# Performance work log

Hardware: AMD Instinct MI355X
Metric: run time of the kernel (lower is better)

Reference implementation:

```python
import jax, jax.numpy as jnp
import numpy as np

B, N, C = 2, 2048, 1024
H = 16
D = C // H
HID = 4 * C
EPS = 1e-5


def layernorm(x, g, b):
    mu = jnp.mean(x, axis=-1, keepdims=True)
    var = jnp.var(x, axis=-1, keepdims=True)
    return (x - mu) * jax.lax.rsqrt(var + EPS) * g + b


def setup_inputs() -> dict:
    key = jax.random.key(0)
    ks = jax.random.split(key, 8)
    s = lambda fan_in: 1.0 / np.sqrt(fan_in)
    return {
        "x": jax.random.normal(ks[0], (B, N, C), dtype=jnp.float32),
        "ln1_g": jnp.ones((C,), jnp.float32),
        "ln1_b": jnp.zeros((C,), jnp.float32),
        "w_qkv": jax.random.normal(ks[1], (C, 3 * C), jnp.float32) * s(C),
        "w_proj": jax.random.normal(ks[2], (C, C), jnp.float32) * s(C),
        "b_proj": jnp.zeros((C,), jnp.float32),
        "ln2_g": jnp.ones((C,), jnp.float32),
        "ln2_b": jnp.zeros((C,), jnp.float32),
        "w_fc1": jax.random.normal(ks[3], (C, HID), jnp.float32) * s(C),
        "b_fc1": jnp.zeros((HID,), jnp.float32),
        "w_fc2": jax.random.normal(ks[4], (HID, C), jnp.float32) * s(HID),
        "b_fc2": jnp.zeros((C,), jnp.float32),
        "metadata": 0,
        "thw_shape": 2048,
    }


def reference(x, ln1_g, ln1_b, w_qkv, w_proj, b_proj, ln2_g, ln2_b,
              w_fc1, b_fc1, w_fc2, b_fc2, metadata, thw_shape):
    scale = 1.0 / np.sqrt(D)
    # --- attention branch (pre-norm) ---
    xn = layernorm(x, ln1_g, ln1_b)
    qkv = (xn @ w_qkv).reshape(B, N, 3, H, D)
    q = jnp.transpose(qkv[:, :, 0], (0, 2, 1, 3))  # [B,H,N,D]
    k = jnp.transpose(qkv[:, :, 1], (0, 2, 1, 3))
    v = jnp.transpose(qkv[:, :, 2], (0, 2, 1, 3))
    attn = jax.nn.softmax(jnp.einsum('bhnd,bhmd->bhnm', q, k) * scale, axis=-1)
    o = jnp.einsum('bhnm,bhmd->bhnd', attn, v)
    o = jnp.transpose(o, (0, 2, 1, 3)).reshape(B, N, C)
    x = x + (o @ w_proj + b_proj)
    # --- MLP branch (pre-norm) ---
    xn2 = layernorm(x, ln2_g, ln2_b)
    h = jax.nn.gelu(xn2 @ w_fc1 + b_fc1, approximate=False)  # torch GELU = exact erf
    x = x + (h @ w_fc2 + b_fc2)
    return x
```

## Files before the change

kernel.cpp:

```cpp
#include <hip/hip_runtime.h>

#define B_   2
#define N_   2048
#define C_   1024
#define H_   16
#define D_   64
#define HID_ 4096
#define M_   (B_ * N_)

typedef __attribute__((ext_vector_type(8))) short bf16x8;
typedef __attribute__((ext_vector_type(4))) short short4v;
typedef __attribute__((ext_vector_type(4))) float f32x4;

__device__ __forceinline__ unsigned short f2bf(float f) {
  unsigned int u = __builtin_bit_cast(unsigned int, f);
  u += 0x7fffu + ((u >> 16) & 1u);
  return (unsigned short)(u >> 16);
}

__device__ __forceinline__ void gl2lds16(const void* g, void* l) {
  __builtin_amdgcn_global_load_lds(
      (const __attribute__((address_space(1))) unsigned int*)g,
      (__attribute__((address_space(3))) unsigned int*)l, 16, 0, 0);
}

__global__ __launch_bounds__(256) void ln_kernel(const float* __restrict__ x,
                                                 const float* __restrict__ g,
                                                 const float* __restrict__ bta,
                                                 unsigned short* __restrict__ out) {
  int row  = blockIdx.x * 4 + (threadIdx.x >> 6);
  int lane = threadIdx.x & 63;
  const float* xr = x + (size_t)row * C_;
  float4 v[4];
  float s1 = 0.f, s2 = 0.f;
#pragma unroll
  for (int j = 0; j < 4; j++) {
    v[j] = *(const float4*)(xr + j * 256 + lane * 4);
    s1 += v[j].x + v[j].y + v[j].z + v[j].w;
    s2 += v[j].x * v[j].x + v[j].y * v[j].y + v[j].z * v[j].z + v[j].w * v[j].w;
  }
#pragma unroll
  for (int m = 1; m < 64; m <<= 1) { s1 += __shfl_xor(s1, m); s2 += __shfl_xor(s2, m); }
  float mu  = s1 * (1.0f / C_);
  float var = s2 * (1.0f / C_) - mu * mu;
  float rs  = rsqrtf(var + 1e-5f);
#pragma unroll
  for (int j = 0; j < 4; j++) {
    const float4 gv = *(const float4*)(g + j * 256 + lane * 4);
    const float4 bv = *(const float4*)(bta + j * 256 + lane * 4);
    ushort4 o;
    o.x = f2bf((v[j].x - mu) * rs * gv.x + bv.x);
    o.y = f2bf((v[j].y - mu) * rs * gv.y + bv.y);
    o.z = f2bf((v[j].z - mu) * rs * gv.z + bv.z);
    o.w = f2bf((v[j].w - mu) * rs * gv.w + bv.w);
    *(ushort4*)(out + (size_t)row * C_ + j * 256 + lane * 4) = o;
  }
}

__global__ __launch_bounds__(256) void wtrans_kernel(const float* __restrict__ W,
                                                     unsigned short* __restrict__ Wt,
                                                     int K, int N) {
  __shared__ float t[32][33];
  int n0 = blockIdx.x * 32, k0 = blockIdx.y * 32;
  int tx = threadIdx.x, ty = threadIdx.y;
#pragma unroll
  for (int j = 0; j < 4; j++)
    t[ty + j * 8][tx] = W[(size_t)(k0 + ty + j * 8) * N + n0 + tx];
  __syncthreads();
#pragma unroll
  for (int j = 0; j < 4; j++)
    Wt[(size_t)(n0 + ty + j * 8) * K + k0 + tx] = f2bf(t[tx][ty + j * 8]);
}

__global__ __launch_bounds__(256) void vtrans_kernel(const unsigned short* __restrict__ v,
                                                     unsigned short* __restrict__ vt) {
  __shared__ unsigned short t[32][33];
  int bh = blockIdx.z;
  int n0 = blockIdx.x * 32, d0 = blockIdx.y * 32;
  const unsigned short* src = v + (size_t)bh * N_ * D_;
  unsigned short* dst = vt + (size_t)bh * D_ * N_;
  int tx = threadIdx.x, ty = threadIdx.y;
#pragma unroll
  for (int j = 0; j < 4; j++)
    t[ty + j * 8][tx] = src[(size_t)(n0 + ty + j * 8) * D_ + d0 + tx];
  __syncthreads();
#pragma unroll
  for (int j = 0; j < 4; j++)
    dst[(size_t)(d0 + ty + j * 8) * N_ + n0 + tx] = t[tx][ty + j * 8];
}

template <int MODE, int BN>
__global__ __launch_bounds__(256) void gemm_kernel(
    const unsigned short* __restrict__ A,
    const unsigned short* __restrict__ Wt,
    const float* __restrict__ bias,
    const float* __restrict__ resid,
    float* __restrict__ outf,
    unsigned short* __restrict__ outb0,
    unsigned short* __restrict__ outb1,
    unsigned short* __restrict__ outb2,
    int M, int N, int K) {
  constexpr int MT = (BN == 128) ? 4 : 2;
  __shared__ __align__(16) short As[128][64];
  __shared__ __align__(16) short Bs[BN][64];
  int tid = threadIdx.x;
  int w = tid >> 6, lane = tid & 63, r = lane & 15, quad = lane >> 4;
  int rowbase = (BN == 128) ? (w >> 1) * 64 : w * 32;
  int colbase = (BN == 128) ? (w & 1) * 64 : 0;
  int bM = blockIdx.y * 128, bN = blockIdx.x * BN;

  int srow   = (w << 3) + (lane >> 3);
  int schunk = (lane & 7) ^ ((lane >> 3) & 7);
  const unsigned short* aP = A  + (size_t)(bM + srow) * K + schunk * 8;
  const unsigned short* bP = Wt + (size_t)(bN + srow) * K + schunk * 8;

  int pc0 = (quad ^ (r & 7)) * 8;

  f32x4 acc[MT][4];
#pragma unroll
  for (int i = 0; i < MT; i++)
#pragma unroll
    for (int j = 0; j < 4; j++) acc[i][j] = f32x4{0.f, 0.f, 0.f, 0.f};

  for (int k0 = 0; k0 < K; k0 += 64) {
    __syncthreads();
#pragma unroll
    for (int p = 0; p < 4; p++)
      gl2lds16(aP + (size_t)(p * 32) * K + k0, &As[p * 32 + (w << 3)][0]);
#pragma unroll
    for (int p = 0; p < BN / 32; p++)
      gl2lds16(bP + (size_t)(p * 32) * K + k0, &Bs[p * 32 + (w << 3)][0]);
    __syncthreads();
#pragma unroll
    for (int kh = 0; kh < 2; kh++) {
      int pc = pc0 ^ (kh * 32);
      bf16x8 af[MT], bfr[4];
#pragma unroll
      for (int mt = 0; mt < MT; mt++)
        af[mt] = *(const bf16x8*)&As[rowbase + mt * 16 + r][pc];
#pragma unroll
      for (int nt = 0; nt < 4; nt++)
        bfr[nt] = *(const bf16x8*)&Bs[colbase + nt * 16 + r][pc];
#pragma unroll
      for (int mt = 0; mt < MT; mt++)
#pragma unroll
        for (int nt = 0; nt < 4; nt++)
          acc[mt][nt] = __builtin_amdgcn_mfma_f32_16x16x32_bf16(af[mt], bfr[nt], acc[mt][nt], 0, 0, 0);
    }
  }

#pragma unroll
  for (int mt = 0; mt < MT; mt++) {
#pragma unroll
    for (int nt = 0; nt < 4; nt++) {
#pragma unroll
      for (int i = 0; i < 4; i++) {
        int gm = bM + rowbase + mt * 16 + quad * 4 + i;
        int gn = bN + colbase + nt * 16 + r;
        float val = acc[mt][nt][i];
        if (MODE == 0) {
          int s = gn >> 10, c = gn & 1023;
          int hh = c >> 6, d = c & 63;
          int b = gm >> 11, n = gm & 2047;
          size_t di = ((size_t)(b * H_ + hh) * N_ + n) * D_ + d;
          unsigned short bvv = f2bf(s == 0 ? val * 0.125f : val);
          (s == 0 ? outb0 : (s == 1 ? outb1 : outb2))[di] = bvv;
        } else if (MODE == 1) {
          outf[(size_t)gm * N + gn] = val + bias[gn] + resid[(size_t)gm * N + gn];
        } else {
          float t = val + bias[gn];
          float gl = 0.5f * t * (1.0f + erff(t * 0.70710678118f));
          outb0[(size_t)gm * N + gn] = f2bf(gl);
        }
      }
    }
  }
}

__global__ __launch_bounds__(256) void attn_kernel(const unsigned short* __restrict__ qb,
                                                   const unsigned short* __restrict__ kb,
                                                   const unsigned short* __restrict__ vtb,
                                                   unsigned short* __restrict__ ob) {
  __shared__ __align__(16) short Ks[128][64];
  __shared__ __align__(16) short Vts[64][128];
  int tid = threadIdx.x;
  int w = tid >> 6, lane = tid & 63, r = lane & 15, quad = lane >> 4;
  int bh = blockIdx.x >> 4, qt = blockIdx.x & 15;
  const unsigned short* qh  = qb  + (size_t)bh * N_ * D_;
  const unsigned short* kh  = kb  + (size_t)bh * N_ * D_;
  const unsigned short* vth = vtb + (size_t)bh * D_ * N_;

  bf16x8 qf[2][2];
#pragma unroll
  for (int mt = 0; mt < 2; mt++)
#pragma unroll
    for (int ks = 0; ks < 2; ks++)
      qf[mt][ks] = *(const bf16x8*)(qh + (size_t)(qt * 128 + w * 32 + mt * 16 + r) * D_ + ks * 32 + quad * 8);

  float mst[2] = {-1e30f, -1e30f}, lst[2] = {0.f, 0.f};
  f32x4 oacc[2][4];
#pragma unroll
  for (int mt = 0; mt < 2; mt++)
#pragma unroll
    for (int nt = 0; nt < 4; nt++) oacc[mt][nt] = f32x4{0.f, 0.f, 0.f, 0.f};

  int krow   = (w << 3) + (lane >> 3);
  int kchunk = (lane & 7) ^ ((lane >> 3) & 7);
  const unsigned short* kP = kh + (size_t)krow * D_ + kchunk * 8;
  int vrow   = (w << 2) + (lane >> 4);
  int vchunk = (lane & 15) ^ (vrow & 7);
  const unsigned short* vP = vth + (size_t)vrow * N_ + vchunk * 8;

  short* Plw = &Ks[0][0] + w * 2048;
  int swz = (r & 7);

  for (int t = 0; t < 16; t++) {
    __syncthreads();
#pragma unroll
    for (int p = 0; p < 4; p++)
      gl2lds16(kP + (size_t)(t * 128 + p * 32) * D_, &Ks[p * 32 + (w << 3)][0]);
#pragma unroll
    for (int p = 0; p < 4; p++)
      gl2lds16(vP + (size_t)(p * 16) * N_ + t * 128, &Vts[p * 16 + (w << 2)][0]);
    __syncthreads();

    f32x4 sacc[2][8];
#pragma unroll
    for (int mt = 0; mt < 2; mt++)
#pragma unroll
      for (int nt = 0; nt < 8; nt++) sacc[mt][nt] = f32x4{0.f, 0.f, 0.f, 0.f};
#pragma unroll
    for (int ks = 0; ks < 2; ks++) {
#pragma unroll
      for (int nt = 0; nt < 8; nt++) {
        bf16x8 kfr = *(const bf16x8*)&Ks[nt * 16 + r][((ks * 4 + quad) ^ swz) * 8];
#pragma unroll
        for (int mt = 0; mt < 2; mt++)
          sacc[mt][nt] = __builtin_amdgcn_mfma_f32_16x16x32_bf16(kfr, qf[mt][ks], sacc[mt][nt], 0, 0, 0);
      }
    }

    float alpha[2];
#pragma unroll
    for (int mt = 0; mt < 2; mt++) {
      float tm = -1e30f;
#pragma unroll
      for (int nt = 0; nt < 8; nt++)
#pragma unroll
        for (int i = 0; i < 4; i++) tm = fmaxf(tm, sacc[mt][nt][i]);
      tm = fmaxf(tm, __shfl_xor(tm, 16));
      tm = fmaxf(tm, __shfl_xor(tm, 32));
      float mnew = fmaxf(mst[mt], tm);
      alpha[mt] = __expf(mst[mt] - mnew);
      mst[mt] = mnew;
      float rs = 0.f;
#pragma unroll
      for (int nt = 0; nt < 8; nt++)
#pragma unroll
        for (int i = 0; i < 4; i++) {
          float p = __expf(sacc[mt][nt][i] - mnew);
          sacc[mt][nt][i] = p;
          rs += p;
        }
      rs += __shfl_xor(rs, 16);
      rs += __shfl_xor(rs, 32);
      lst[mt] = lst[mt] * alpha[mt] + rs;
#pragma unroll
      for (int i = 0; i < 4; i++) {
        float av = __shfl(alpha[mt], (lane & 48) | (quad * 4 + i));
#pragma unroll
        for (int nt = 0; nt < 4; nt++) oacc[mt][nt][i] *= av;
      }
    }

    __syncthreads();

#pragma unroll
    for (int mt = 0; mt < 2; mt++) {
#pragma unroll
      for (int nt = 0; nt < 8; nt++) {
        short4v pk;
        pk[0] = (short)f2bf(sacc[mt][nt][0]);
        pk[1] = (short)f2bf(sacc[mt][nt][1]);
        pk[2] = (short)f2bf(sacc[mt][nt][2]);
        pk[3] = (short)f2bf(sacc[mt][nt][3]);
        *(short4v*)&Plw[r * 128 + (((nt * 2 + (quad >> 1)) ^ swz) * 8) + (quad & 1) * 4] = pk;
      }
      asm volatile("" ::: "memory");
#pragma unroll
      for (int ks = 0; ks < 4; ks++) {
        bf16x8 pfr = *(const bf16x8*)&Plw[r * 128 + ((ks * 4 + quad) ^ swz) * 8];
#pragma unroll
        for (int nt2 = 0; nt2 < 4; nt2++) {
          bf16x8 vfr = *(const bf16x8*)&Vts[nt2 * 16 + r][((ks * 4 + quad) ^ swz) * 8];
          oacc[mt][nt2] = __builtin_amdgcn_mfma_f32_16x16x32_bf16(pfr, vfr, oacc[mt][nt2], 0, 0, 0);
        }
      }
      asm volatile("" ::: "memory");
    }
  }

  int bb = bh >> 4, hh = bh & 15;
#pragma unroll
  for (int mt = 0; mt < 2; mt++) {
#pragma unroll
    for (int i = 0; i < 4; i++) {
      float li = __shfl(lst[mt], (lane & 48) | (quad * 4 + i));
      float inv = 1.0f / li;
      int row = qt * 128 + w * 32 + mt * 16 + quad * 4 + i;
#pragma unroll
      for (int nt2 = 0; nt2 < 4; nt2++) {
        int d = nt2 * 16 + r;
        ob[((size_t)bb * N_ + row) * C_ + hh * D_ + d] = f2bf(oacc[mt][nt2][i] * inv);
      }
    }
  }
}

extern "C" void kernel_launch(void* const* d_in, const int* in_sizes, int n_in,
                              void* d_out, int out_size, void* d_ws, size_t ws_size,
                              hipStream_t stream) {
  const float* x     = (const float*)d_in[0];
  const float* ln1g  = (const float*)d_in[1];
  const float* ln1b  = (const float*)d_in[2];
  const float* wqkv  = (const float*)d_in[3];
  const float* wproj = (const float*)d_in[4];
  const float* bproj = (const float*)d_in[5];
  const float* ln2g  = (const float*)d_in[6];
  const float* ln2b  = (const float*)d_in[7];
  const float* wfc1  = (const float*)d_in[8];
  const float* bfc1  = (const float*)d_in[9];
  const float* wfc2  = (const float*)d_in[10];
  const float* bfc2  = (const float*)d_in[11];
  float* out = (float*)d_out;

  const size_t MB = 1u << 20;
  if (ws_size < 88 * MB) return;
  char* w = (char*)d_ws;
  unsigned short* xn    = (unsigned short*)(w + 0 * MB);
  unsigned short* qbuf  = (unsigned short*)(w + 8 * MB);
  unsigned short* kbuf  = (unsigned short*)(w + 16 * MB);
  unsigned short* vbuf  = (unsigned short*)(w + 24 * MB);
  unsigned short* hbuf  = (unsigned short*)(w + 0 * MB);
  unsigned short* obuf  = (unsigned short*)(w + 32 * MB);
  float*          x2    = (float*)         (w + 40 * MB);
  unsigned short* xn2   = (unsigned short*)(w + 56 * MB);
  unsigned short* vtb   = (unsigned short*)(w + 56 * MB);
  unsigned short* wqkvt = (unsigned short*)(w + 64 * MB);
  unsigned short* wprjt = (unsigned short*)(w + 70 * MB);
  unsigned short* wfc1t = (unsigned short*)(w + 72 * MB);
  unsigned short* wfc2t = (unsigned short*)(w + 80 * MB);

  dim3 tb(32, 8);
  ln_kernel<<<M_ / 4, 256, 0, stream>>>(x, ln1g, ln1b, xn);
  wtrans_kernel<<<dim3(3 * C_ / 32, C_ / 32), tb, 0, stream>>>(wqkv, wqkvt, C_, 3 * C_);
  wtrans_kernel<<<dim3(C_ / 32, C_ / 32), tb, 0, stream>>>(wproj, wprjt, C_, C_);
  wtrans_kernel<<<dim3(HID_ / 32, C_ / 32), tb, 0, stream>>>(wfc1, wfc1t, C_, HID_);
  wtrans_kernel<<<dim3(C_ / 32, HID_ / 32), tb, 0, stream>>>(wfc2, wfc2t, HID_, C_);

  gemm_kernel<0, 128><<<dim3(3 * C_ / 128, M_ / 128), 256, 0, stream>>>(
      xn, wqkvt, nullptr, nullptr, nullptr, qbuf, kbuf, vbuf, M_, 3 * C_, C_);
  vtrans_kernel<<<dim3(N_ / 32, D_ / 32, B_ * H_), tb, 0, stream>>>(vbuf, vtb);
  attn_kernel<<<B_ * H_ * (N_ / 128), 256, 0, stream>>>(qbuf, kbuf, vtb, obuf);
  gemm_kernel<1, 64><<<dim3(C_ / 64, M_ / 128), 256, 0, stream>>>(
      obuf, wprjt, bproj, x, x2, nullptr, nullptr, nullptr, M_, C_, C_);
  ln_kernel<<<M_ / 4, 256, 0, stream>>>(x2, ln2g, ln2b, xn2);
  gemm_kernel<2, 128><<<dim3(HID_ / 128, M_ / 128), 256, 0, stream>>>(
      xn2, wfc1t, bfc1, nullptr, nullptr, hbuf, nullptr, nullptr, M_, HID_, C_);
  gemm_kernel<1, 64><<<dim3(C_ / 64, M_ / 128), 256, 0, stream>>>(
      hbuf, wfc2t, bfc2, x2, out, nullptr, nullptr, nullptr, M_, C_, HID_);
}
```

Baseline: 385.1 us.

## Split attention KV range and FC2 K dimension across blocks for more parallelism

Attention now splits each query tile's key range into two halves processed by separate blocks. Each block writes a normalized partial output plus its running max and sum, and a new combine kernel merges the halves with log-sum-exp weights. The FC2 GEMM switches to 128-wide tiles with a two-way split-K; one half writes bias plus residual and the other writes a partial buffer that a separate add kernel folds in. Both changes aim to fill more CUs on a grid that was small (512 attention blocks, 512 FC2 blocks), at the cost of extra kernel launches, intermediate traffic, and an extra bf16 rounding of the partial attention outputs.

```diff
diff --git a/kernel.cpp b/kernel.cpp
--- a/kernel.cpp
+++ b/kernel.cpp
@@ -16,6 +16,10 @@
   unsigned int u = __builtin_bit_cast(unsigned int, f);
   u += 0x7fffu + ((u >> 16) & 1u);
   return (unsigned short)(u >> 16);
+}
+__device__ __forceinline__ float bf2f(unsigned short s) {
+  unsigned int u = ((unsigned int)s) << 16;
+  return __builtin_bit_cast(float, u);
 }
 
 __device__ __forceinline__ void gl2lds16(const void* g, void* l) {
@@ -96,6 +100,7 @@
     const float* __restrict__ bias,
     const float* __restrict__ resid,
     float* __restrict__ outf,
+    float* __restrict__ partf,
     unsigned short* __restrict__ outb0,
     unsigned short* __restrict__ outb1,
     unsigned short* __restrict__ outb2,
@@ -109,6 +114,10 @@
   int colbase = (BN == 128) ? (w & 1) * 64 : 0;
   int bM = blockIdx.y * 128, bN = blockIdx.x * BN;
 
+  int kz   = (MODE == 3) ? blockIdx.z : 0;
+  int kbeg = (MODE == 3) ? kz * (K >> 1) : 0;
+  int kend = (MODE == 3) ? kbeg + (K >> 1) : K;
+
   int srow   = (w << 3) + (lane >> 3);
   int schunk = (lane & 7) ^ ((lane >> 3) & 7);
   const unsigned short* aP = A  + (size_t)(bM + srow) * K + schunk * 8;
@@ -122,7 +131,7 @@
 #pragma unroll
     for (int j = 0; j < 4; j++) acc[i][j] = f32x4{0.f, 0.f, 0.f, 0.f};
 
-  for (int k0 = 0; k0 < K; k0 += 64) {
+  for (int k0 = kbeg; k0 < kend; k0 += 64) {
     __syncthreads();
 #pragma unroll
     for (int p = 0; p < 4; p++)
@@ -167,25 +176,42 @@
           (s == 0 ? outb0 : (s == 1 ? outb1 : outb2))[di] = bvv;
         } else if (MODE == 1) {
           outf[(size_t)gm * N + gn] = val + bias[gn] + resid[(size_t)gm * N + gn];
-        } else {
+        } else if (MODE == 2) {
           float t = val + bias[gn];
           float gl = 0.5f * t * (1.0f + erff(t * 0.70710678118f));
           outb0[(size_t)gm * N + gn] = f2bf(gl);
+        } else {
+          if (kz == 0)
+            outf[(size_t)gm * N + gn] = val + bias[gn] + resid[(size_t)gm * N + gn];
+          else
+            partf[(size_t)gm * N + gn] = val;
         }
       }
     }
   }
 }
 
-__global__ __launch_bounds__(256) void attn_kernel(const unsigned short* __restrict__ qb,
-                                                   const unsigned short* __restrict__ kb,
-                                                   const unsigned short* __restrict__ vtb,
-                                                   unsigned short* __restrict__ ob) {
+__global__ __launch_bounds__(256) void addpart_kernel(float* __restrict__ out,
+                                                      const float* __restrict__ part) {
+  int i = blockIdx.x * 256 + threadIdx.x;
+  float4 a = *(const float4*)(out + (size_t)i * 4);
+  float4 b = *(const float4*)(part + (size_t)i * 4);
+  a.x += b.x; a.y += b.y; a.z += b.z; a.w += b.w;
+  *(float4*)(out + (size_t)i * 4) = a;
+}
+
+__global__ __launch_bounds__(256, 4) void attn_kernel(const unsigned short* __restrict__ qb,
+                                                      const unsigned short* __restrict__ kb,
+                                                      const unsigned short* __restrict__ vtb,
+                                                      unsigned short* __restrict__ Op,
+                                                      float2* __restrict__ ml) {
   __shared__ __align__(16) short Ks[128][64];
   __shared__ __align__(16) short Vts[64][128];
   int tid = threadIdx.x;
   int w = tid >> 6, lane = tid & 63, r = lane & 15, quad = lane >> 4;
-  int bh = blockIdx.x >> 4, qt = blockIdx.x & 15;
+  int kbi = blockIdx.x & 1;
+  int idx = blockIdx.x >> 1;
+  int bh = idx >> 4, qt = idx & 15;
   const unsigned short* qh  = qb  + (size_t)bh * N_ * D_;
   const unsigned short* kh  = kb  + (size_t)bh * N_ * D_;
   const unsigned short* vth = vtb + (size_t)bh * D_ * N_;
@@ -214,7 +240,7 @@
   short* Plw = &Ks[0][0] + w * 2048;
   int swz = (r & 7);
 
-  for (int t = 0; t < 16; t++) {
+  for (int t = kbi * 8; t < kbi * 8 + 8; t++) {
     __syncthreads();
 #pragma unroll
     for (int p = 0; p < 4; p++)
@@ -300,9 +326,13 @@
     }
   }
 
-  int bb = bh >> 4, hh = bh & 15;
+  size_t base = ((size_t)(kbi * 32 + bh)) * N_;
 #pragma unroll
   for (int mt = 0; mt < 2; mt++) {
+    if (quad == 0) {
+      int row = qt * 128 + w * 32 + mt * 16 + r;
+      ml[base + row] = float2{mst[mt], lst[mt]};
+    }
 #pragma unroll
     for (int i = 0; i < 4; i++) {
       float li = __shfl(lst[mt], (lane & 48) | (quad * 4 + i));
@@ -311,10 +341,43 @@
 #pragma unroll
       for (int nt2 = 0; nt2 < 4; nt2++) {
         int d = nt2 * 16 + r;
-        ob[((size_t)bb * N_ + row) * C_ + hh * D_ + d] = f2bf(oacc[mt][nt2][i] * inv);
-      }
-    }
-  }
+        Op[(base + row) * D_ + d] = f2bf(oacc[mt][nt2][i] * inv);
+      }
+    }
+  }
+}
+
+__global__ __launch_bounds__(256) void attn_combine_kernel(const unsigned short* __restrict__ Op,
+                                                           const float2* __restrict__ ml,
+                                                           unsigned short* __restrict__ ob) {
+  int gid = blockIdx.x * 256 + threadIdx.x;
+  int row = gid >> 3;
+  int dq  = (gid & 7) << 3;
+  int bh = row >> 11, n = row & 2047;
+  int bb = bh >> 4, hh = bh & 15;
+  float2 a0 = ml[row];
+  float2 a1 = ml[(size_t)B_ * H_ * N_ + row];
+  float m = fmaxf(a0.x, a1.x);
+  float w0 = __expf(a0.x - m) * a0.y;
+  float w1 = __expf(a1.x - m) * a1.y;
+  float inv = 1.0f / (w0 + w1);
+  w0 *= inv; w1 *= inv;
+  const ushort4 o0  = *(const ushort4*)(Op + (size_t)row * D_ + dq);
+  const ushort4 o0b = *(const ushort4*)(Op + (size_t)row * D_ + dq + 4);
+  const ushort4 o1  = *(const ushort4*)(Op + ((size_t)B_ * H_ * N_ + row) * D_ + dq);
+  const ushort4 o1b = *(const ushort4*)(Op + ((size_t)B_ * H_ * N_ + row) * D_ + dq + 4);
+  ushort4 r0, r1;
+  r0.x = f2bf(w0 * bf2f(o0.x) + w1 * bf2f(o1.x));
+  r0.y = f2bf(w0 * bf2f(o0.y) + w1 * bf2f(o1.y));
+  r0.z = f2bf(w0 * bf2f(o0.z) + w1 * bf2f(o1.z));
+  r0.w = f2bf(w0 * bf2f(o0.w) + w1 * bf2f(o1.w));
+  r1.x = f2bf(w0 * bf2f(o0b.x) + w1 * bf2f(o1b.x));
+  r1.y = f2bf(w0 * bf2f(o0b.y) + w1 * bf2f(o1b.y));
+  r1.z = f2bf(w0 * bf2f(o0b.z) + w1 * bf2f(o1b.z));
+  r1.w = f2bf(w0 * bf2f(o0b.w) + w1 * bf2f(o1b.w));
+  unsigned short* dst = ob + ((size_t)bb * N_ + n) * C_ + hh * D_ + dq;
+  *(ushort4*)dst = r0;
+  *(ushort4*)(dst + 4) = r1;
 }
 
 extern "C" void kernel_launch(void* const* d_in, const int* in_sizes, int n_in,
@@ -338,15 +401,18 @@
   if (ws_size < 88 * MB) return;
   char* w = (char*)d_ws;
   unsigned short* xn    = (unsigned short*)(w + 0 * MB);
+  float2*         mlbuf = (float2*)        (w + 0 * MB);
   unsigned short* qbuf  = (unsigned short*)(w + 8 * MB);
   unsigned short* kbuf  = (unsigned short*)(w + 16 * MB);
   unsigned short* vbuf  = (unsigned short*)(w + 24 * MB);
   unsigned short* hbuf  = (unsigned short*)(w + 0 * MB);
   unsigned short* obuf  = (unsigned short*)(w + 32 * MB);
   float*          x2    = (float*)         (w + 40 * MB);
+  unsigned short* opart = (unsigned short*)(w + 40 * MB);
   unsigned short* xn2   = (unsigned short*)(w + 56 * MB);
   unsigned short* vtb   = (unsigned short*)(w + 56 * MB);
   unsigned short* wqkvt = (unsigned short*)(w + 64 * MB);
+  float*          partf = (float*)         (w + 64 * MB);
   unsigned short* wprjt = (unsigned short*)(w + 70 * MB);
   unsigned short* wfc1t = (unsigned short*)(w + 72 * MB);
   unsigned short* wfc2t = (unsigned short*)(w + 80 * MB);
@@ -359,14 +425,16 @@
   wtrans_kernel<<<dim3(C_ / 32, HID_ / 32), tb, 0, stream>>>(wfc2, wfc2t, HID_, C_);
 
   gemm_kernel<0, 128><<<dim3(3 * C_ / 128, M_ / 128), 256, 0, stream>>>(
-      xn, wqkvt, nullptr, nullptr, nullptr, qbuf, kbuf, vbuf, M_, 3 * C_, C_);
+      xn, wqkvt, nullptr, nullptr, nullptr, nullptr, qbuf, kbuf, vbuf, M_, 3 * C_, C_);
   vtrans_kernel<<<dim3(N_ / 32, D_ / 32, B_ * H_), tb, 0, stream>>>(vbuf, vtb);
-  attn_kernel<<<B_ * H_ * (N_ / 128), 256, 0, stream>>>(qbuf, kbuf, vtb, obuf);
+  attn_kernel<<<B_ * H_ * (N_ / 128) * 2, 256, 0, stream>>>(qbuf, kbuf, vtb, opart, mlbuf);
+  attn_combine_kernel<<<B_ * H_ * N_ * 8 / 256, 256, 0, stream>>>(opart, mlbuf, obuf);
   gemm_kernel<1, 64><<<dim3(C_ / 64, M_ / 128), 256, 0, stream>>>(
-      obuf, wprjt, bproj, x, x2, nullptr, nullptr, nullptr, M_, C_, C_);
+      obuf, wprjt, bproj, x, x2, nullptr, nullptr, nullptr, nullptr, M_, C_, C_);
   ln_kernel<<<M_ / 4, 256, 0, stream>>>(x2, ln2g, ln2b, xn2);
   gemm_kernel<2, 128><<<dim3(HID_ / 128, M_ / 128), 256, 0, stream>>>(
-      xn2, wfc1t, bfc1, nullptr, nullptr, hbuf, nullptr, nullptr, M_, HID_, C_);
-  gemm_kernel<1, 64><<<dim3(C_ / 64, M_ / 128), 256, 0, stream>>>(
-      hbuf, wfc2t, bfc2, x2, out, nullptr, nullptr, nullptr, M_, C_, HID_);
-}
+      xn2, wfc1t, bfc1, nullptr, nullptr, nullptr, hbuf, nullptr, nullptr, M_, HID_, C_);
+  gemm_kernel<3, 128><<<dim3(C_ / 128, M_ / 128, 2), 256, 0, stream>>>(
+      hbuf, wfc2t, bfc2, x2, out, partf, nullptr, nullptr, nullptr, M_, C_, HID_);
+  addpart_kernel<<<M_ * C_ / 1024, 256, 0, stream>>>(out, partf);
+}
```

Measured after the change: 505.9 us. 1.31x slower.
